# Kernel optimization log

Measured on AMD Instinct MI355X. Metric: run time of the kernel, lower is better.

The kernel has to match this reference:

```python
import jax, jax.numpy as jnp
import numpy as np

N_HEADS = 16
ROPE_BASE = 10000.0

def apply_rope(x):
    # x: [B, H, S, D] with D even; interleaved-pair RoPE (torchtune style)
    B, H, S, D = x.shape
    half = D // 2
    inv_freq = 1.0 / (ROPE_BASE ** (jnp.arange(0, half, dtype=jnp.float32) / half))
    angles = jnp.arange(S, dtype=jnp.float32)[:, None] * inv_freq[None, :]  # [S, D/2]
    cos = jnp.cos(angles)[None, None]  # [1,1,S,D/2]
    sin = jnp.sin(angles)[None, None]
    x1 = x[..., 0::2]
    x2 = x[..., 1::2]
    r1 = x1 * cos - x2 * sin
    r2 = x1 * sin + x2 * cos
    return jnp.stack([r1, r2], axis=-1).reshape(B, H, S, D)

def setup_inputs() -> dict:
    key = jax.random.key(0)
    ks = jax.random.split(key, 5)
    B, S, E = 2, 2048, 1024
    d_attn = 1024
    scale = 1.0 / np.sqrt(E)
    x = jax.random.normal(ks[0], (B, S, E), dtype=jnp.float32)
    Wq = jax.random.normal(ks[1], (d_attn, E), dtype=jnp.float32) * scale
    Wk = jax.random.normal(ks[2], (d_attn, E), dtype=jnp.float32) * scale
    Wv = jax.random.normal(ks[3], (d_attn, E), dtype=jnp.float32) * scale
    Wo = jax.random.normal(ks[4], (E, d_attn), dtype=jnp.float32) * scale
    return {"x": x, "Wq": Wq, "Wk": Wk, "Wv": Wv, "Wo": Wo}

def reference(x, Wq, Wk, Wv, Wo):
    B, S, E = x.shape
    d_attn = Wq.shape[0]
    hd = d_attn // N_HEADS
    attn_scale = 1.0 / np.sqrt(d_attn)
    # projections (nn.Linear: x @ W.T), split heads -> [B, H, S, hd]
    q = (x @ Wq.T).reshape(B, S, N_HEADS, hd).transpose(0, 2, 1, 3)
    k = (x @ Wk.T).reshape(B, S, N_HEADS, hd).transpose(0, 2, 1, 3)
    v = (x @ Wv.T).reshape(B, S, N_HEADS, hd).transpose(0, 2, 1, 3)
    q = apply_rope(q)
    k = apply_rope(k)
    scores = jnp.einsum('bhqd,bhkd->bhqk', q, k) * attn_scale  # [B,H,S,S]
    causal = jnp.tril(jnp.ones((S, S), dtype=bool))
    scores = jnp.where(causal[None, None], scores, -jnp.inf)
    probs = jax.nn.softmax(scores, axis=-1)  # dropout is identity in eval
    out = jnp.einsum('bhqk,bhkd->bhqd', probs, v)
    out = out.transpose(0, 2, 1, 3).reshape(B, S, d_attn)
    return out @ Wo.T
```

## Files before the change

### kernel.cpp

```cpp
#include <hip/hip_runtime.h>


typedef float  f32x4  __attribute__((ext_vector_type(4)));
typedef short  short8 __attribute__((ext_vector_type(8)));

#define MFMA16(a,b,c) __builtin_amdgcn_mfma_f32_16x16x32_bf16((a),(b),(c),0,0,0)
#define GLD_LDS16(g, l)                                                        \
  __builtin_amdgcn_global_load_lds(                                            \
      (const __attribute__((address_space(1))) unsigned int*)(g),              \
      (__attribute__((address_space(3))) unsigned int*)(l), 16, 0, 0)

__device__ __forceinline__ unsigned short f2bf(float f) {
  unsigned int x = __float_as_uint(f);
  x += 0x7fffu + ((x >> 16) & 1u);
  return (unsigned short)(x >> 16);
}
__device__ __forceinline__ float bf2f(unsigned short u) {
  return __uint_as_float(((unsigned int)u) << 16);
}

__global__ __launch_bounds__(256) void cvt_all(const float* __restrict__ x,
                                               const float* __restrict__ wq,
                                               const float* __restrict__ wk,
                                               const float* __restrict__ wv,
                                               const float* __restrict__ wo,
                                               ushort* __restrict__ dst) {
  const int i = blockIdx.x * 256 + threadIdx.x;
  const float* src;
  int off;
  if (i < 1048576) { src = x; off = i; }
  else {
    const int j = i - 1048576;
    const int wsel = j >> 18;
    off = j & 262143;
    src = (wsel == 0) ? wq : (wsel == 1) ? wk : (wsel == 2) ? wv : wo;
  }
  const float4 v = ((const float4*)src)[off];
  ushort4 o = make_ushort4(f2bf(v.x), f2bf(v.y), f2bf(v.z), f2bf(v.w));
  ((ushort4*)dst)[i] = o;
}

template<int MODE, int BN, int BM>
__global__ __launch_bounds__(256) void gemm_bt(const ushort* __restrict__ A,
                                               const ushort* __restrict__ B,
                                               void* __restrict__ Cv,
                                               int K) {
  constexpr int NI = BN / 32;
  constexpr int MI = BM / 32;
  constexpr int AI = BM / 64;
  constexpr int BI = BN / 64;
  __shared__ __align__(16) short As0[BM * 32];
  __shared__ __align__(16) short As1[BM * 32];
  __shared__ __align__(16) short Bs0[BN * 32];
  __shared__ __align__(16) short Bs1[BN * 32];
  const int tid  = threadIdx.x;
  const int lane = tid & 63, w = tid >> 6;
  const int ln   = lane & 15, quad = lane >> 4;
  const int wm   = w >> 1, wn = w & 1;
  const int m0 = blockIdx.y * BM, n0 = blockIdx.x * BN;

  const int srow = lane >> 2;
  const int schk = (lane & 3) * 8;
  const int arow = w * (16 * AI);
  const int brow = w * (16 * BI);
  const ushort* Ag0 = A + (size_t)(m0 + arow + srow) * K + schk;
  const ushort* Ag1 = A + (size_t)(m0 + arow + 16 + srow) * K + schk;
  const ushort* Bg0 = B + (size_t)(n0 + brow + srow) * K + schk;
  const ushort* Bg1 = B + (size_t)(n0 + brow + 16 + srow) * K + schk;
  const int lA0 = arow * 32, lA1 = (arow + 16) * 32;
  const int lB0 = brow * 32, lB1 = (brow + 16) * 32;

  int aoff[MI], boff[NI];
#pragma unroll
  for (int i = 0; i < MI; i++)
    aoff[i] = (wm * (BM / 2) + i * 16 + ln) * 32 + quad * 8;
#pragma unroll
  for (int i = 0; i < NI; i++)
    boff[i] = (wn * (BN / 2) + i * 16 + ln) * 32 + quad * 8;
  f32x4 acc[MI][NI] = {};

  for (int kt = 0; kt < K; kt += 64) {
    __syncthreads();
    GLD_LDS16(Ag0 + kt, As0 + lA0);
    if (AI == 2) GLD_LDS16(Ag1 + kt, As0 + lA1);
    GLD_LDS16(Ag0 + kt + 32, As1 + lA0);
    if (AI == 2) GLD_LDS16(Ag1 + kt + 32, As1 + lA1);
    GLD_LDS16(Bg0 + kt, Bs0 + lB0);
    if (BI == 2) GLD_LDS16(Bg1 + kt, Bs0 + lB1);
    GLD_LDS16(Bg0 + kt + 32, Bs1 + lB0);
    if (BI == 2) GLD_LDS16(Bg1 + kt + 32, Bs1 + lB1);
    __syncthreads();
#pragma unroll
    for (int h = 0; h < 2; ++h) {
      const short* Ap = h ? As1 : As0;
      const short* Bp = h ? Bs1 : Bs0;
      short8 av[MI], bv[NI];
#pragma unroll
      for (int i = 0; i < MI; i++) av[i] = *(const short8*)&Ap[aoff[i]];
#pragma unroll
      for (int i = 0; i < NI; i++) bv[i] = *(const short8*)&Bp[boff[i]];
#pragma unroll
      for (int mi = 0; mi < MI; mi++)
#pragma unroll
        for (int ni = 0; ni < NI; ni++)
          acc[mi][ni] = MFMA16(av[mi], bv[ni], acc[mi][ni]);
    }
  }

  if (MODE == 0) {
    ushort* Cq = (ushort*)Cv;
    if (n0 < 2048) {
      ushort* dst = Cq + (n0 < 1024 ? 0 : 4194304);
      const int nbase = (n0 < 1024) ? n0 : n0 - 1024;
      const float qsc = (n0 < 1024) ? 0.04508422002778011f : 1.0f;
      const float sgn = (ln & 1) ? 1.0f : -1.0f;
      float invc[NI];
#pragma unroll
      for (int ni = 0; ni < NI; ni++) {
        const int ii = ((wn * (BN / 2) + ni * 16 + ln) & 63) >> 1;
        invc[ni] = __builtin_amdgcn_exp2f(-(float)ii * 0.4152410118579865f) *
                   0.15915494309189535f;
      }
#pragma unroll
      for (int mi = 0; mi < MI; mi++) {
        const int row = m0 + wm * (BM / 2) + mi * 16 + quad * 4;
#pragma unroll
        for (int ni = 0; ni < NI; ni++) {
          const int col = nbase + wn * (BN / 2) + ni * 16 + ln;
#pragma unroll
          for (int r = 0; r < 4; r++) {
            const float mine  = acc[mi][ni][r];
            const float other = __shfl_xor(mine, 1, 64);
            const int   s     = (row + r) & 2047;
            const float rev   = (float)s * invc[ni];
            const float rr    = rev - floorf(rev);
            const float sn = __builtin_amdgcn_sinf(rr);
            const float cs = __builtin_amdgcn_cosf(rr);
            const float rot = (mine * cs + sgn * other * sn) * qsc;
            dst[(size_t)(row + r) * 1024 + col] = f2bf(rot);
          }
        }
      }
    } else {
      ushort* vt = Cq + 8388608;
#pragma unroll
      for (int mi = 0; mi < MI; mi++) {
        const int sm = m0 + wm * (BM / 2) + mi * 16 + quad * 4;
        const int b = sm >> 11, s = sm & 2047;
#pragma unroll
        for (int ni = 0; ni < NI; ni++) {
          const int nv = (n0 - 2048) + wn * (BN / 2) + ni * 16 + ln;
          const int bh = b * 16 + (nv >> 6), d = nv & 63;
          ushort4 u = make_ushort4(f2bf(acc[mi][ni][0]), f2bf(acc[mi][ni][1]),
                                   f2bf(acc[mi][ni][2]), f2bf(acc[mi][ni][3]));
          *(ushort4*)&vt[((size_t)bh * 64 + d) * 2048 + s] = u;
        }
      }
    }
  } else {
    float* C = (float*)Cv;
#pragma unroll
    for (int mi = 0; mi < MI; mi++) {
      const int row = m0 + wm * (BM / 2) + mi * 16 + quad * 4;
#pragma unroll
      for (int ni = 0; ni < NI; ni++) {
        const int col = n0 + wn * (BN / 2) + ni * 16 + ln;
#pragma unroll
        for (int r = 0; r < 4; r++)
          C[(size_t)(row + r) * 1024 + col] = acc[mi][ni][r];
      }
    }
  }
}

__global__ __launch_bounds__(256) void attnk(const ushort* __restrict__ q,
                                             const ushort* __restrict__ k,
                                             const ushort* __restrict__ vt,
                                             ushort* __restrict__ ctx) {
  __shared__ __align__(16) short Ks[64 * 72];
  __shared__ __align__(16) short Vs[64 * 72];
  __shared__ __align__(16) short Ps[4 * 16 * 72];
  const int tid  = threadIdx.x;
  const int lane = tid & 63, w = tid >> 6;
  const int ln   = lane & 15, quad = lane >> 4;
  const int x = blockIdx.x, bh = blockIdx.y;
  const int b = bh >> 4, h = bh & 15;
  const int jA = x, jB = 31 - x;
  short* Pw = Ps + w * 1152;

  const size_t qbA = ((size_t)(b * 2048 + jA * 64 + w * 16 + ln)) * 1024 + h * 64;
  const size_t qbB = ((size_t)(b * 2048 + jB * 64 + w * 16 + ln)) * 1024 + h * 64;
  const short8 aqA0 = *(const short8*)&q[qbA + quad * 8];
  const short8 aqA1 = *(const short8*)&q[qbA + 32 + quad * 8];
  const short8 aqB0 = *(const short8*)&q[qbB + quad * 8];
  const short8 aqB1 = *(const short8*)&q[qbB + 32 + quad * 8];

  f32x4 oA[4] = {}, oB[4] = {};
  float lsA[4] = {0.f, 0.f, 0.f, 0.f}, lsB[4] = {0.f, 0.f, 0.f, 0.f};

  const int s0 = tid, s1 = tid + 256;
  const int r0 = s0 >> 3, c0 = (s0 & 7) * 8;
  const int r1 = s1 >> 3, c1 = (s1 & 7) * 8;
  const ushort* kg0 = k  + ((size_t)(b * 2048 + r0)) * 1024 + h * 64 + c0;
  const ushort* kg1 = k  + ((size_t)(b * 2048 + r1)) * 1024 + h * 64 + c1;
  const ushort* vg0 = vt + ((size_t)(bh * 64 + r0)) * 2048 + c0;
  const ushort* vg1 = vt + ((size_t)(bh * 64 + r1)) * 2048 + c1;
  const int wK0 = r0 * 72 + c0, wK1 = r1 * 72 + c1;

  short8 kr0 = *(const short8*)(kg0);
  short8 kr1 = *(const short8*)(kg1);
  short8 vr0 = *(const short8*)(vg0);
  short8 vr1 = *(const short8*)(vg1);

  for (int t = 0; t <= jB; t++) {
    __syncthreads();
    *(short8*)&Ks[wK0] = kr0;
    *(short8*)&Ks[wK1] = kr1;
    *(short8*)&Vs[wK0] = vr0;
    *(short8*)&Vs[wK1] = vr1;
    if (t < jB) {
      kr0 = *(const short8*)(kg0 + (size_t)(t + 1) * 65536);
      kr1 = *(const short8*)(kg1 + (size_t)(t + 1) * 65536);
      vr0 = *(const short8*)(vg0 + (t + 1) * 64);
      vr1 = *(const short8*)(vg1 + (t + 1) * 64);
    }
    asm volatile("s_waitcnt lgkmcnt(0)" ::: "memory");
    __builtin_amdgcn_s_barrier();
    __builtin_amdgcn_sched_barrier(0);

    const bool actA = (t <= jA);
    f32x4 scA[4], scB[4];
#pragma unroll
    for (int ct = 0; ct < 4; ct++) {
      const short8 bk0 = *(const short8*)&Ks[(ct * 16 + ln) * 72 + quad * 8];
      const short8 bk1 = *(const short8*)&Ks[(ct * 16 + ln) * 72 + 32 + quad * 8];
      f32x4 z = {0.f, 0.f, 0.f, 0.f};
      z = MFMA16(aqB0, bk0, z);
      z = MFMA16(aqB1, bk1, z);
      scB[ct] = z;
      if (actA) {
        f32x4 y = {0.f, 0.f, 0.f, 0.f};
        y = MFMA16(aqA0, bk0, y);
        y = MFMA16(aqA1, bk1, y);
        scA[ct] = y;
      }
    }
    if (t == jB) {
#pragma unroll
      for (int ct = 0; ct < 4; ct++) {
        const int kv = (t << 6) + ct * 16 + ln;
#pragma unroll
        for (int r = 0; r < 4; r++)
          if (kv > jB * 64 + w * 16 + quad * 4 + r) scB[ct][r] = -100000.0f;
      }
    }
    if (actA && t == jA) {
#pragma unroll
      for (int ct = 0; ct < 4; ct++) {
        const int kv = (t << 6) + ct * 16 + ln;
#pragma unroll
        for (int r = 0; r < 4; r++)
          if (kv > jA * 64 + w * 16 + quad * 4 + r) scA[ct][r] = -100000.0f;
      }
    }

    short8 bv0[4], bv1[4];
#pragma unroll
    for (int dt = 0; dt < 4; dt++) {
      bv0[dt] = *(const short8*)&Vs[(dt * 16 + ln) * 72 + quad * 8];
      bv1[dt] = *(const short8*)&Vs[(dt * 16 + ln) * 72 + 32 + quad * 8];
    }

#pragma unroll
    for (int ct = 0; ct < 4; ct++)
#pragma unroll
      for (int r = 0; r < 4; r++) {
        const float p = __builtin_amdgcn_exp2f(scB[ct][r]);
        lsB[r] += p;
        Pw[(quad * 4 + r) * 72 + ct * 16 + ln] = (short)f2bf(p);
      }
    {
      const short8 ap0 = *(const short8*)&Pw[ln * 72 + quad * 8];
      const short8 ap1 = *(const short8*)&Pw[ln * 72 + 32 + quad * 8];
#pragma unroll
      for (int dt = 0; dt < 4; dt++) {
        oB[dt] = MFMA16(ap0, bv0[dt], oB[dt]);
        oB[dt] = MFMA16(ap1, bv1[dt], oB[dt]);
      }
    }
    if (actA) {
#pragma unroll
      for (int ct = 0; ct < 4; ct++)
#pragma unroll
        for (int r = 0; r < 4; r++) {
          const float p = __builtin_amdgcn_exp2f(scA[ct][r]);
          lsA[r] += p;
          Pw[(quad * 4 + r) * 72 + ct * 16 + ln] = (short)f2bf(p);
        }
      const short8 ap0 = *(const short8*)&Pw[ln * 72 + quad * 8];
      const short8 ap1 = *(const short8*)&Pw[ln * 72 + 32 + quad * 8];
#pragma unroll
      for (int dt = 0; dt < 4; dt++) {
        oA[dt] = MFMA16(ap0, bv0[dt], oA[dt]);
        oA[dt] = MFMA16(ap1, bv1[dt], oA[dt]);
      }
    }
  }

#pragma unroll
  for (int off = 1; off < 16; off <<= 1)
#pragma unroll
    for (int r = 0; r < 4; r++) {
      lsA[r] += __shfl_xor(lsA[r], off, 64);
      lsB[r] += __shfl_xor(lsB[r], off, 64);
    }

#pragma unroll
  for (int r = 0; r < 4; r++) {
    const float invA = 1.0f / lsA[r];
    const float invB = 1.0f / lsB[r];
    const int rowA = jA * 64 + w * 16 + quad * 4 + r;
    const int rowB = jB * 64 + w * 16 + quad * 4 + r;
#pragma unroll
    for (int dt = 0; dt < 4; dt++) {
      ctx[((size_t)(b * 2048 + rowA)) * 1024 + h * 64 + dt * 16 + ln] =
          f2bf(oA[dt][r] * invA);
      ctx[((size_t)(b * 2048 + rowB)) * 1024 + h * 64 + dt * 16 + ln] =
          f2bf(oB[dt][r] * invB);
    }
  }
}

extern "C" void kernel_launch(void* const* d_in, const int* in_sizes, int n_in,
                              void* d_out, int out_size, void* d_ws, size_t ws_size,
                              hipStream_t stream) {
  const float* x  = (const float*)d_in[0];
  const float* Wq = (const float*)d_in[1];
  const float* Wk = (const float*)d_in[2];
  const float* Wv = (const float*)d_in[3];
  const float* Wo = (const float*)d_in[4];
  float* out = (float*)d_out;
  char* ws = (char*)d_ws;

  ushort* xb  = (ushort*)(ws);
  ushort* wqb = (ushort*)(ws + (size_t)(8  << 20));
  ushort* qb  = (ushort*)(ws + (size_t)(16 << 20));
  ushort* kb  = (ushort*)(ws + (size_t)(24 << 20));
  ushort* vtb = (ushort*)(ws + (size_t)(32 << 20));
  ushort* ctx = (ushort*)(ws + (size_t)(40 << 20));

  cvt_all<<<8192, 256, 0, stream>>>(x, Wq, Wk, Wv, Wo, xb);
  gemm_bt<0, 64, 128><<<dim3(48, 32), 256, 0, stream>>>(xb, wqb, (void*)qb, 1024);
  attnk<<<dim3(16, 32), 256, 0, stream>>>(qb, kb, vtb, ctx);
  gemm_bt<2, 64, 64><<<dim3(16, 64), 256, 0, stream>>>(ctx, wqb + 3145728 , (void*)out, 1024);
}
```

Baseline: 187.4 us.

## Double-buffer K/V tiles in LDS and split P scratch per query block

Adds a second LDS buffer for the K and V tiles. Each iteration writes the next tile into the alternate buffer and issues global loads two tiles ahead, which removes the extra barrier and lgkmcnt wait before compute. The P scratch is split into separate A and B buffers so the two softmax/PV passes do not reuse the same LDS region. The cost is roughly double the LDS footprint, which may lower occupancy, and the prefetched values stay live in registers across a whole iteration.

```diff
diff --git a/kernel.cpp b/kernel.cpp
--- a/kernel.cpp
+++ b/kernel.cpp
@@ -177,16 +177,18 @@
                                              const ushort* __restrict__ k,
                                              const ushort* __restrict__ vt,
                                              ushort* __restrict__ ctx) {
-  __shared__ __align__(16) short Ks[64 * 72];
-  __shared__ __align__(16) short Vs[64 * 72];
-  __shared__ __align__(16) short Ps[4 * 16 * 72];
+  __shared__ __align__(16) short Ks[2][64 * 72];
+  __shared__ __align__(16) short Vs[2][64 * 72];
+  __shared__ __align__(16) short PsB[4 * 16 * 72];
+  __shared__ __align__(16) short PsA[4 * 16 * 72];
   const int tid  = threadIdx.x;
   const int lane = tid & 63, w = tid >> 6;
   const int ln   = lane & 15, quad = lane >> 4;
   const int x = blockIdx.x, bh = blockIdx.y;
   const int b = bh >> 4, h = bh & 15;
   const int jA = x, jB = 31 - x;
-  short* Pw = Ps + w * 1152;
+  short* PwB = PsB + w * 1152;
+  short* PwA = PsA + w * 1152;
 
   const size_t qbA = ((size_t)(b * 2048 + jA * 64 + w * 16 + ln)) * 1024 + h * 64;
   const size_t qbB = ((size_t)(b * 2048 + jB * 64 + w * 16 + ln)) * 1024 + h * 64;
@@ -211,29 +213,40 @@
   short8 kr1 = *(const short8*)(kg1);
   short8 vr0 = *(const short8*)(vg0);
   short8 vr1 = *(const short8*)(vg1);
+  *(short8*)&Ks[0][wK0] = kr0;
+  *(short8*)&Ks[0][wK1] = kr1;
+  *(short8*)&Vs[0][wK0] = vr0;
+  *(short8*)&Vs[0][wK1] = vr1;
+  kr0 = *(const short8*)(kg0 + 65536);
+  kr1 = *(const short8*)(kg1 + 65536);
+  vr0 = *(const short8*)(vg0 + 64);
+  vr1 = *(const short8*)(vg1 + 64);
 
   for (int t = 0; t <= jB; t++) {
     __syncthreads();
-    *(short8*)&Ks[wK0] = kr0;
-    *(short8*)&Ks[wK1] = kr1;
-    *(short8*)&Vs[wK0] = vr0;
-    *(short8*)&Vs[wK1] = vr1;
+    const short* Kc = Ks[t & 1];
+    const short* Vc = Vs[t & 1];
     if (t < jB) {
-      kr0 = *(const short8*)(kg0 + (size_t)(t + 1) * 65536);
-      kr1 = *(const short8*)(kg1 + (size_t)(t + 1) * 65536);
-      vr0 = *(const short8*)(vg0 + (t + 1) * 64);
-      vr1 = *(const short8*)(vg1 + (t + 1) * 64);
-    }
-    asm volatile("s_waitcnt lgkmcnt(0)" ::: "memory");
-    __builtin_amdgcn_s_barrier();
-    __builtin_amdgcn_sched_barrier(0);
+      short* Kn = (short*)Ks[(t & 1) ^ 1];
+      short* Vn = (short*)Vs[(t & 1) ^ 1];
+      *(short8*)&Kn[wK0] = kr0;
+      *(short8*)&Kn[wK1] = kr1;
+      *(short8*)&Vn[wK0] = vr0;
+      *(short8*)&Vn[wK1] = vr1;
+    }
+    if (t + 2 <= jB) {
+      kr0 = *(const short8*)(kg0 + (size_t)(t + 2) * 65536);
+      kr1 = *(const short8*)(kg1 + (size_t)(t + 2) * 65536);
+      vr0 = *(const short8*)(vg0 + (t + 2) * 64);
+      vr1 = *(const short8*)(vg1 + (t + 2) * 64);
+    }
 
     const bool actA = (t <= jA);
     f32x4 scA[4], scB[4];
 #pragma unroll
     for (int ct = 0; ct < 4; ct++) {
-      const short8 bk0 = *(const short8*)&Ks[(ct * 16 + ln) * 72 + quad * 8];
-      const short8 bk1 = *(const short8*)&Ks[(ct * 16 + ln) * 72 + 32 + quad * 8];
+      const short8 bk0 = *(const short8*)&Kc[(ct * 16 + ln) * 72 + quad * 8];
+      const short8 bk1 = *(const short8*)&Kc[(ct * 16 + ln) * 72 + 32 + quad * 8];
       f32x4 z = {0.f, 0.f, 0.f, 0.f};
       z = MFMA16(aqB0, bk0, z);
       z = MFMA16(aqB1, bk1, z);
@@ -267,8 +280,8 @@
     short8 bv0[4], bv1[4];
 #pragma unroll
     for (int dt = 0; dt < 4; dt++) {
-      bv0[dt] = *(const short8*)&Vs[(dt * 16 + ln) * 72 + quad * 8];
-      bv1[dt] = *(const short8*)&Vs[(dt * 16 + ln) * 72 + 32 + quad * 8];
+      bv0[dt] = *(const short8*)&Vc[(dt * 16 + ln) * 72 + quad * 8];
+      bv1[dt] = *(const short8*)&Vc[(dt * 16 + ln) * 72 + 32 + quad * 8];
     }
 
 #pragma unroll
@@ -277,11 +290,11 @@
       for (int r = 0; r < 4; r++) {
         const float p = __builtin_amdgcn_exp2f(scB[ct][r]);
         lsB[r] += p;
-        Pw[(quad * 4 + r) * 72 + ct * 16 + ln] = (short)f2bf(p);
+        PwB[(quad * 4 + r) * 72 + ct * 16 + ln] = (short)f2bf(p);
       }
     {
-      const short8 ap0 = *(const short8*)&Pw[ln * 72 + quad * 8];
-      const short8 ap1 = *(const short8*)&Pw[ln * 72 + 32 + quad * 8];
+      const short8 ap0 = *(const short8*)&PwB[ln * 72 + quad * 8];
+      const short8 ap1 = *(const short8*)&PwB[ln * 72 + 32 + quad * 8];
 #pragma unroll
       for (int dt = 0; dt < 4; dt++) {
         oB[dt] = MFMA16(ap0, bv0[dt], oB[dt]);
@@ -295,10 +308,10 @@
         for (int r = 0; r < 4; r++) {
           const float p = __builtin_amdgcn_exp2f(scA[ct][r]);
           lsA[r] += p;
-          Pw[(quad * 4 + r) * 72 + ct * 16 + ln] = (short)f2bf(p);
+          PwA[(quad * 4 + r) * 72 + ct * 16 + ln] = (short)f2bf(p);
         }
-      const short8 ap0 = *(const short8*)&Pw[ln * 72 + quad * 8];
-      const short8 ap1 = *(const short8*)&Pw[ln * 72 + 32 + quad * 8];
+      const short8 ap0 = *(const short8*)&PwA[ln * 72 + quad * 8];
+      const short8 ap1 = *(const short8*)&PwA[ln * 72 + 32 + quad * 8];
 #pragma unroll
       for (int dt = 0; dt < 4; dt++) {
         oA[dt] = MFMA16(ap0, bv0[dt], oA[dt]);
```

New measurement: 186.4 us. No clear change (-0.5%).
